# Kernel tuning notes

Hardware: AMD Instinct MI355X
Metric: run time of the kernel (lower is better)

Reference implementation:

```python
import jax, jax.numpy as jnp
import numpy as np

H = 2048      # hidden_size
E = 16        # num_experts
I = 512       # moe_intermediate_size
IS = 2048     # shared_expert_intermediate_size
TOP_K = 2
B, S = 1, 2048


def setup_inputs() -> dict:
    key = jax.random.key(0)
    ks = jax.random.split(key, 9)
    std = 0.02
    return {
        "hidden_states": jax.random.normal(ks[0], (B, S, H), dtype=jnp.float32),
        "gate_w": jax.random.normal(ks[1], (E, H), dtype=jnp.float32) * std,
        "w1": jax.random.normal(ks[2], (E, I, H), dtype=jnp.float32) * std,  # gate_proj per expert
        "w2": jax.random.normal(ks[3], (E, H, I), dtype=jnp.float32) * std,  # down_proj per expert
        "w3": jax.random.normal(ks[4], (E, I, H), dtype=jnp.float32) * std,  # up_proj per expert
        "ws_gate": jax.random.normal(ks[5], (IS, H), dtype=jnp.float32) * std,  # shared gate_proj
        "ws_up": jax.random.normal(ks[6], (IS, H), dtype=jnp.float32) * std,    # shared up_proj
        "ws_down": jax.random.normal(ks[7], (H, IS), dtype=jnp.float32) * std,  # shared down_proj
        "shared_gate_w": jax.random.normal(ks[8], (1, H), dtype=jnp.float32) * std,
    }


def reference(hidden_states, gate_w, w1, w2, w3, ws_gate, ws_up, ws_down, shared_gate_w):
    b, s, h = hidden_states.shape
    x = hidden_states.reshape(-1, h)                     # [T, H]
    T = x.shape[0]

    # Router: softmax in fp32, top-k, renormalize (norm_topk_prob=True)
    router_logits = x @ gate_w.T                         # [T, E]
    routing = jax.nn.softmax(router_logits.astype(jnp.float32), axis=-1)
    topw, sel = jax.lax.top_k(routing, TOP_K)            # [T, K]
    topw = topw / jnp.sum(topw, axis=-1, keepdims=True)
    topw = topw.astype(x.dtype)

    # Scatter top-k weights into dense [T, E] combine matrix (torch_moe semantics)
    combine = jnp.zeros((T, E), dtype=x.dtype).at[jnp.arange(T)[:, None], sel].set(topw)

    # Expert SwiGLU MLPs evaluated densely, masked/weighted by combine
    hmid = jax.nn.silu(jnp.einsum('th,eih->tei', x, w1)) * jnp.einsum('th,eih->tei', x, w3)  # [T,E,I]
    hmid = hmid * combine[:, :, None]
    moe_out = jnp.einsum('tei,ehi->th', hmid, w2)        # [T, H]

    # Shared expert with sigmoid gate
    shared = (jax.nn.silu(x @ ws_gate.T) * (x @ ws_up.T)) @ ws_down.T  # [T, H]
    shared = jax.nn.sigmoid(x @ shared_gate_w.T) * shared

    return (moe_out + shared).reshape(b, s, h)
```

## Files before the change

kernel.cpp:

```cpp
#include <hip/hip_runtime.h>
#include <hip/hip_bf16.h>
#include <cmath>

#define HDIM 2048
#define NEXP 16
#define IDIM 512
#define ISDIM 2048
#define NTOK 2048
#define MAXTILES 80
#define ROWSCAP (MAXTILES * 64)
#define NB_EXP 640
#define NB_SH 1024

typedef short bf16x8 __attribute__((ext_vector_type(8)));
typedef float f32x4 __attribute__((ext_vector_type(4)));

__device__ __forceinline__ unsigned short f2bf(float f) {
  unsigned int u = __builtin_bit_cast(unsigned int, f);
  u += 0x7FFFu + ((u >> 16) & 1u);
  return (unsigned short)(u >> 16);
}

__device__ __forceinline__ void stage_w8(const float* __restrict__ src,
                                         unsigned short* __restrict__ dst) {
  const float4* p = reinterpret_cast<const float4*>(src);
  float4 a = p[0];
  float4 b = p[1];
  bf16x8 v = {(short)f2bf(a.x), (short)f2bf(a.y), (short)f2bf(a.z), (short)f2bf(a.w),
              (short)f2bf(b.x), (short)f2bf(b.y), (short)f2bf(b.z), (short)f2bf(b.w)};
  *reinterpret_cast<bf16x8*>(dst) = v;
}

__global__ __launch_bounds__(256) void k_router(const float* __restrict__ x,
                                                const float* __restrict__ gate_w,
                                                const float* __restrict__ sgw,
                                                unsigned short* __restrict__ xb,
                                                int* __restrict__ sel,
                                                float* __restrict__ wnorm,
                                                float* __restrict__ sig,
                                                int* __restrict__ counts) {
  __shared__ float lg[4][17];
  int tid = threadIdx.x, wid = tid >> 6, lane = tid & 63;
  int t = blockIdx.x * 4 + wid;
  const float4* xrow = reinterpret_cast<const float4*>(x + (size_t)t * HDIM);
  float4 xv[8];
#pragma unroll
  for (int s = 0; s < 8; s++) xv[s] = xrow[s * 64 + lane];
  ushort4* xbrow = reinterpret_cast<ushort4*>(xb + (size_t)t * HDIM);
#pragma unroll
  for (int s = 0; s < 8; s++) {
    ushort4 o;
    o.x = f2bf(xv[s].x); o.y = f2bf(xv[s].y); o.z = f2bf(xv[s].z); o.w = f2bf(xv[s].w);
    xbrow[s * 64 + lane] = o;
  }
#pragma unroll 1
  for (int e = 0; e < 17; e++) {
    const float4* gr =
        reinterpret_cast<const float4*>(e < 16 ? gate_w + (size_t)e * HDIM : sgw);
    float acc = 0.f;
#pragma unroll
    for (int s = 0; s < 8; s++) {
      float4 g = gr[s * 64 + lane];
      acc += xv[s].x * g.x + xv[s].y * g.y + xv[s].z * g.z + xv[s].w * g.w;
    }
#pragma unroll
    for (int off = 32; off; off >>= 1) acc += __shfl_xor(acc, off, 64);
    if (lane == 0) lg[wid][e] = acc;
  }
  if (lane == 0) {
    float* L = lg[wid];
    int i1 = 0; float v1 = L[0];
    for (int i = 1; i < NEXP; i++) if (L[i] > v1) { v1 = L[i]; i1 = i; }
    int i2 = (i1 == 0) ? 1 : 0; float v2 = L[i2];
    for (int i = 0; i < NEXP; i++)
      if (i != i1 && i != i2 && L[i] > v2) { v2 = L[i]; i2 = i; }
    float wa = 1.f / (1.f + expf(v2 - v1));
    sel[2 * t] = i1; sel[2 * t + 1] = i2;
    wnorm[2 * t] = wa; wnorm[2 * t + 1] = 1.f - wa;
    sig[t] = 1.f / (1.f + expf(-L[16]));
    atomicAdd(&counts[i1], 1);
    atomicAdd(&counts[i2], 1);
  }
}

__global__ __launch_bounds__(256) void k_scan_scatter(const int* __restrict__ counts,
                                                      const int* __restrict__ sel,
                                                      int* __restrict__ tile_expert,
                                                      int* __restrict__ row_token,
                                                      int* __restrict__ tok2row) {
  __shared__ int offs_s[NEXP];
  __shared__ int fill_s[NEXP];
  int tid = threadIdx.x;
  for (int r = tid; r < ROWSCAP; r += 256) row_token[r] = -1;
  if (tid < NEXP) fill_s[tid] = 0;
  if (tid == 0) {
    int acc = 0;
    for (int e = 0; e < NEXP; e++) {
      offs_s[e] = acc;
      int nt = (counts[e] + 63) >> 6;
      for (int i = 0; i < nt; i++) tile_expert[(acc >> 6) + i] = e;
      acc += nt << 6;
    }
    for (int m = acc >> 6; m < MAXTILES; m++) tile_expert[m] = -1;
  }
  __syncthreads();
  for (int t = tid; t < NTOK; t += 256) {
    for (int k = 0; k < 2; k++) {
      int e = sel[2 * t + k];
      int pos = atomicAdd(&fill_s[e], 1);
      int row = offs_s[e] + pos;
      row_token[row] = t;
      tok2row[2 * t + k] = row;
    }
  }
}

__global__ __launch_bounds__(256) void k_gu(
    const unsigned short* __restrict__ xb, const float* __restrict__ w1,
    const float* __restrict__ w3, const float* __restrict__ wsg,
    const float* __restrict__ wsu, const int* __restrict__ tile_expert,
    const int* __restrict__ row_token, unsigned short* __restrict__ hmid,
    unsigned short* __restrict__ hs) {
  __shared__ unsigned short As[64 * 72];
  __shared__ unsigned short Bg[64 * 72];
  __shared__ unsigned short Bu[64 * 72];
  __shared__ int toks[64];
  int bid = blockIdx.x, tid = threadIdx.x;
  const float *bGp, *bUp;
  unsigned short* outp;
  int ostride, mt, ncol;
  if (bid < NB_EXP) {
    mt = bid >> 3;
    int nt = bid & 7;
    int e = tile_expert[mt];
    if (e < 0) return;
    if (tid < 64) {
      int tk = row_token[mt * 64 + tid];
      toks[tid] = tk < 0 ? 0 : tk;
    }
    bGp = w1 + ((size_t)e * IDIM + nt * 64) * HDIM;
    bUp = w3 + ((size_t)e * IDIM + nt * 64) * HDIM;
    outp = hmid; ostride = IDIM; ncol = nt * 64;
  } else {
    int sb = bid - NB_EXP;
    mt = sb >> 5;
    int nt = sb & 31;
    if (tid < 64) toks[tid] = mt * 64 + tid;
    bGp = wsg + (size_t)(nt * 64) * HDIM;
    bUp = wsu + (size_t)(nt * 64) * HDIM;
    outp = hs; ostride = ISDIM; ncol = nt * 64;
  }
  int wave = tid >> 6, lane = tid & 63;
  int wm = wave >> 1, wn = wave & 1;
  int quad = lane >> 4, l16 = lane & 15;
  int r0 = tid >> 3, kof0 = (tid & 7) << 3;
  int c2 = tid + 256;
  int r1 = c2 >> 3, kof1 = (c2 & 7) << 3;
  f32x4 accG[2][2] = {};
  f32x4 accU[2][2] = {};
  __syncthreads();
  for (int k0 = 0; k0 < HDIM; k0 += 64) {
    *reinterpret_cast<bf16x8*>(&As[r0 * 72 + kof0]) =
        *reinterpret_cast<const bf16x8*>(xb + (size_t)toks[r0] * HDIM + k0 + kof0);
    *reinterpret_cast<bf16x8*>(&As[r1 * 72 + kof1]) =
        *reinterpret_cast<const bf16x8*>(xb + (size_t)toks[r1] * HDIM + k0 + kof1);
    stage_w8(bGp + (size_t)r0 * HDIM + k0 + kof0, &Bg[r0 * 72 + kof0]);
    stage_w8(bGp + (size_t)r1 * HDIM + k0 + kof1, &Bg[r1 * 72 + kof1]);
    stage_w8(bUp + (size_t)r0 * HDIM + k0 + kof0, &Bu[r0 * 72 + kof0]);
    stage_w8(bUp + (size_t)r1 * HDIM + k0 + kof1, &Bu[r1 * 72 + kof1]);
    __syncthreads();
#pragma unroll
    for (int ks = 0; ks < 2; ks++) {
      bf16x8 af[2], bg[2], bu[2];
#pragma unroll
      for (int ms = 0; ms < 2; ms++)
        af[ms] = *reinterpret_cast<const bf16x8*>(
            &As[(wm * 32 + ms * 16 + l16) * 72 + ks * 32 + quad * 8]);
#pragma unroll
      for (int ns = 0; ns < 2; ns++) {
        bg[ns] = *reinterpret_cast<const bf16x8*>(
            &Bg[(wn * 32 + ns * 16 + l16) * 72 + ks * 32 + quad * 8]);
        bu[ns] = *reinterpret_cast<const bf16x8*>(
            &Bu[(wn * 32 + ns * 16 + l16) * 72 + ks * 32 + quad * 8]);
      }
#pragma unroll
      for (int ms = 0; ms < 2; ms++)
#pragma unroll
        for (int ns = 0; ns < 2; ns++) {
          accG[ms][ns] = __builtin_amdgcn_mfma_f32_16x16x32_bf16(af[ms], bg[ns], accG[ms][ns], 0, 0, 0);
          accU[ms][ns] = __builtin_amdgcn_mfma_f32_16x16x32_bf16(af[ms], bu[ns], accU[ms][ns], 0, 0, 0);
        }
    }
    __syncthreads();
  }
#pragma unroll
  for (int ms = 0; ms < 2; ms++)
#pragma unroll
    for (int ns = 0; ns < 2; ns++)
#pragma unroll
      for (int r = 0; r < 4; r++) {
        float g = accG[ms][ns][r], u = accU[ms][ns][r];
        float hv = (g / (1.f + __expf(-g))) * u;
        int row = mt * 64 + wm * 32 + ms * 16 + quad * 4 + r;
        int col = ncol + wn * 32 + ns * 16 + l16;
        outp[(size_t)row * ostride + col] = f2bf(hv);
      }
}

__global__ __launch_bounds__(256) void k_expert_down(
    const unsigned short* __restrict__ hmid, const float* __restrict__ w2,
    const int* __restrict__ tile_expert, float* __restrict__ moe_rows) {
  int mt = blockIdx.y, nt = blockIdx.x;
  int e = tile_expert[mt];
  if (e < 0) return;
  __shared__ unsigned short As[64 * 72];
  __shared__ unsigned short Bs[64 * 72];
  int tid = threadIdx.x;
  const float* w2e = w2 + ((size_t)e * HDIM + nt * 64) * IDIM;
  int wave = tid >> 6, lane = tid & 63;
  int wm = wave >> 1, wn = wave & 1;
  int quad = lane >> 4, l16 = lane & 15;
  int r0 = tid >> 3, kof0 = (tid & 7) << 3;
  int c2 = tid + 256;
  int r1 = c2 >> 3, kof1 = (c2 & 7) << 3;
  f32x4 acc[2][2] = {};
  for (int k0 = 0; k0 < IDIM; k0 += 64) {
    *reinterpret_cast<bf16x8*>(&As[r0 * 72 + kof0]) =
        *reinterpret_cast<const bf16x8*>(hmid + (size_t)(mt * 64 + r0) * IDIM + k0 + kof0);
    *reinterpret_cast<bf16x8*>(&As[r1 * 72 + kof1]) =
        *reinterpret_cast<const bf16x8*>(hmid + (size_t)(mt * 64 + r1) * IDIM + k0 + kof1);
    stage_w8(w2e + (size_t)r0 * IDIM + k0 + kof0, &Bs[r0 * 72 + kof0]);
    stage_w8(w2e + (size_t)r1 * IDIM + k0 + kof1, &Bs[r1 * 72 + kof1]);
    __syncthreads();
#pragma unroll
    for (int ks = 0; ks < 2; ks++) {
      bf16x8 af[2], bf[2];
#pragma unroll
      for (int ms = 0; ms < 2; ms++)
        af[ms] = *reinterpret_cast<const bf16x8*>(
            &As[(wm * 32 + ms * 16 + l16) * 72 + ks * 32 + quad * 8]);
#pragma unroll
      for (int ns = 0; ns < 2; ns++)
        bf[ns] = *reinterpret_cast<const bf16x8*>(
            &Bs[(wn * 32 + ns * 16 + l16) * 72 + ks * 32 + quad * 8]);
#pragma unroll
      for (int ms = 0; ms < 2; ms++)
#pragma unroll
        for (int ns = 0; ns < 2; ns++)
          acc[ms][ns] = __builtin_amdgcn_mfma_f32_16x16x32_bf16(af[ms], bf[ns], acc[ms][ns], 0, 0, 0);
    }
    __syncthreads();
  }
#pragma unroll
  for (int ms = 0; ms < 2; ms++)
#pragma unroll
    for (int ns = 0; ns < 2; ns++)
#pragma unroll
      for (int r = 0; r < 4; r++) {
        int row = mt * 64 + wm * 32 + ms * 16 + quad * 4 + r;
        int col = nt * 64 + wn * 32 + ns * 16 + l16;
        moe_rows[(size_t)row * HDIM + col] = acc[ms][ns][r];
      }
}

__global__ __launch_bounds__(256) void k_shared_down(
    const unsigned short* __restrict__ hs, const float* __restrict__ wsd,
    const float* __restrict__ moe_rows, const int* __restrict__ tok2row,
    const float* __restrict__ wnorm, const float* __restrict__ sig,
    float* __restrict__ out) {
  int mt = blockIdx.y, nt = blockIdx.x;
  __shared__ unsigned short As[64 * 72];
  __shared__ unsigned short Bs[64 * 72];
  int tid = threadIdx.x;
  const float* wsde = wsd + (size_t)(nt * 64) * ISDIM;
  int wave = tid >> 6, lane = tid & 63;
  int wm = wave >> 1, wn = wave & 1;
  int quad = lane >> 4, l16 = lane & 15;
  int r0 = tid >> 3, kof0 = (tid & 7) << 3;
  int c2 = tid + 256;
  int r1 = c2 >> 3, kof1 = (c2 & 7) << 3;
  f32x4 acc[2][2] = {};
  for (int k0 = 0; k0 < ISDIM; k0 += 64) {
    *reinterpret_cast<bf16x8*>(&As[r0 * 72 + kof0]) =
        *reinterpret_cast<const bf16x8*>(hs + (size_t)(mt * 64 + r0) * ISDIM + k0 + kof0);
    *reinterpret_cast<bf16x8*>(&As[r1 * 72 + kof1]) =
        *reinterpret_cast<const bf16x8*>(hs + (size_t)(mt * 64 + r1) * ISDIM + k0 + kof1);
    stage_w8(wsde + (size_t)r0 * ISDIM + k0 + kof0, &Bs[r0 * 72 + kof0]);
    stage_w8(wsde + (size_t)r1 * ISDIM + k0 + kof1, &Bs[r1 * 72 + kof1]);
    __syncthreads();
#pragma unroll
    for (int ks = 0; ks < 2; ks++) {
      bf16x8 af[2], bf[2];
#pragma unroll
      for (int ms = 0; ms < 2; ms++)
        af[ms] = *reinterpret_cast<const bf16x8*>(
            &As[(wm * 32 + ms * 16 + l16) * 72 + ks * 32 + quad * 8]);
#pragma unroll
      for (int ns = 0; ns < 2; ns++)
        bf[ns] = *reinterpret_cast<const bf16x8*>(
            &Bs[(wn * 32 + ns * 16 + l16) * 72 + ks * 32 + quad * 8]);
#pragma unroll
      for (int ms = 0; ms < 2; ms++)
#pragma unroll
        for (int ns = 0; ns < 2; ns++)
          acc[ms][ns] = __builtin_amdgcn_mfma_f32_16x16x32_bf16(af[ms], bf[ns], acc[ms][ns], 0, 0, 0);
    }
    __syncthreads();
  }
#pragma unroll
  for (int ms = 0; ms < 2; ms++)
#pragma unroll
    for (int ns = 0; ns < 2; ns++)
#pragma unroll
      for (int r = 0; r < 4; r++) {
        int t = mt * 64 + wm * 32 + ms * 16 + quad * 4 + r;
        int col = nt * 64 + wn * 32 + ns * 16 + l16;
        float v = acc[ms][ns][r] * sig[t];
        int ra = tok2row[t * 2], rb = tok2row[t * 2 + 1];
        v += wnorm[t * 2] * moe_rows[(size_t)ra * HDIM + col] +
             wnorm[t * 2 + 1] * moe_rows[(size_t)rb * HDIM + col];
        out[(size_t)t * HDIM + col] = v;
      }
}

extern "C" void kernel_launch(void* const* d_in, const int* in_sizes, int n_in,
                              void* d_out, int out_size, void* d_ws, size_t ws_size,
                              hipStream_t stream) {
  const float* x = (const float*)d_in[0];
  const float* gate_w = (const float*)d_in[1];
  const float* w1 = (const float*)d_in[2];
  const float* w2 = (const float*)d_in[3];
  const float* w3 = (const float*)d_in[4];
  const float* wsg = (const float*)d_in[5];
  const float* wsu = (const float*)d_in[6];
  const float* wsd = (const float*)d_in[7];
  const float* sgw = (const float*)d_in[8];
  float* out = (float*)d_out;

  unsigned short* xb = (unsigned short*)d_ws;
  unsigned short* hs = xb + (size_t)NTOK * HDIM;
  unsigned short* hmid = hs + (size_t)NTOK * ISDIM;
  float* moe_rows = (float*)(hmid + (size_t)ROWSCAP * IDIM);
  float* wnorm = moe_rows + (size_t)ROWSCAP * HDIM;
  float* sig = wnorm + 2 * NTOK;
  int* sel = (int*)(sig + NTOK);
  int* tok2row = sel + 2 * NTOK;
  int* row_token = tok2row + 2 * NTOK;
  int* counts = row_token + ROWSCAP;
  int* tile_expert = counts + NEXP;

  hipMemsetAsync(counts, 0, NEXP * sizeof(int), stream);
  k_router<<<dim3(NTOK / 4), dim3(256), 0, stream>>>(x, gate_w, sgw, xb, sel, wnorm,
                                                     sig, counts);
  k_scan_scatter<<<dim3(1), dim3(256), 0, stream>>>(counts, sel, tile_expert,
                                                    row_token, tok2row);
  k_gu<<<dim3(NB_EXP + NB_SH), dim3(256), 0, stream>>>(xb, w1, w3, wsg, wsu,
                                                       tile_expert, row_token, hmid, hs);
  k_expert_down<<<dim3(HDIM / 64, MAXTILES), dim3(256), 0, stream>>>(
      hmid, w2, tile_expert, moe_rows);
  k_shared_down<<<dim3(HDIM / 64, NTOK / 64), dim3(256), 0, stream>>>(
      hs, wsd, moe_rows, tok2row, wnorm, sig, out);
}
```

Measured before the change: 482.4 us.

## Pre-convert weights to bf16, enlarge GEMM tiles, use direct-to-LDS loads and atomic combine

Adds a kernel that converts all expert and shared weights to bf16 once per call, so the GEMM kernels stop converting fp32 weights during staging and the weights are reread in half the size. The gate/up and down GEMMs get larger N tiles (128 and 256), XOR-swizzled LDS layouts without padding, and global_load_lds for the B operand. Expert-down and shared-down are merged into one kernel that scatters weighted results into a zeroed output with float atomics, removing the moe_rows intermediate buffer. The extra conversion pass reads and writes about 360 MB every call, and the atomics make summation order nondeterministic.

```diff
diff --git a/kernel.cpp b/kernel.cpp
--- a/kernel.cpp
+++ b/kernel.cpp
@@ -9,32 +9,53 @@
 #define NTOK 2048
 #define MAXTILES 80
 #define ROWSCAP (MAXTILES * 64)
-#define NB_EXP 640
-#define NB_SH 1024
+
+#define GU_NBLK_EXP (MAXTILES * 4)
+#define GU_NBLK_SH ((NTOK / 64) * (ISDIM / 128))
+#define DN_NBLK_EXP (MAXTILES * 8)
+#define DN_NBLK_SH ((NTOK / 64) * (HDIM / 256))
 
 typedef short bf16x8 __attribute__((ext_vector_type(8)));
 typedef float f32x4 __attribute__((ext_vector_type(4)));
-
-__device__ __forceinline__ unsigned short f2bf(float f) {
+typedef unsigned short us;
+typedef __attribute__((address_space(1))) const unsigned int* as1p;
+typedef __attribute__((address_space(3))) unsigned int* as3p;
+
+__device__ __forceinline__ us f2bf(float f) {
   unsigned int u = __builtin_bit_cast(unsigned int, f);
   u += 0x7FFFu + ((u >> 16) & 1u);
-  return (unsigned short)(u >> 16);
-}
-
-__device__ __forceinline__ void stage_w8(const float* __restrict__ src,
-                                         unsigned short* __restrict__ dst) {
-  const float4* p = reinterpret_cast<const float4*>(src);
-  float4 a = p[0];
-  float4 b = p[1];
+  return (us)(u >> 16);
+}
+
+__device__ __forceinline__ void glds16(const void* g, void* l) {
+  __builtin_amdgcn_global_load_lds((as1p)(unsigned long long)g,
+                                   (as3p)(unsigned int)(unsigned long long)l, 16, 0, 0);
+}
+
+struct SrcPtrs { const float* p[6]; };
+__global__ __launch_bounds__(256) void k_convert(SrcPtrs s, us* __restrict__ dst) {
+  int b = blockIdx.x;
+  const float* sp;
+  long long rel;
+  size_t doff;
+  if (b < 8192)       { sp = s.p[0]; rel = b;         doff = 0; }
+  else if (b < 16384) { sp = s.p[1]; rel = b - 8192;  doff = 16777216; }
+  else if (b < 24576) { sp = s.p[2]; rel = b - 16384; doff = 33554432; }
+  else if (b < 26624) { sp = s.p[3]; rel = b - 24576; doff = 50331648; }
+  else if (b < 28672) { sp = s.p[4]; rel = b - 26624; doff = 54525952; }
+  else                { sp = s.p[5]; rel = b - 28672; doff = 58720256; }
+  size_t i8 = (size_t)rel * 2048 + threadIdx.x * 8;
+  float4 a = ((const float4*)sp)[i8 >> 2];
+  float4 c = ((const float4*)sp)[(i8 >> 2) + 1];
   bf16x8 v = {(short)f2bf(a.x), (short)f2bf(a.y), (short)f2bf(a.z), (short)f2bf(a.w),
-              (short)f2bf(b.x), (short)f2bf(b.y), (short)f2bf(b.z), (short)f2bf(b.w)};
-  *reinterpret_cast<bf16x8*>(dst) = v;
+              (short)f2bf(c.x), (short)f2bf(c.y), (short)f2bf(c.z), (short)f2bf(c.w)};
+  *(bf16x8*)(dst + doff + i8) = v;
 }
 
 __global__ __launch_bounds__(256) void k_router(const float* __restrict__ x,
                                                 const float* __restrict__ gate_w,
                                                 const float* __restrict__ sgw,
-                                                unsigned short* __restrict__ xb,
+                                                us* __restrict__ xb,
                                                 int* __restrict__ sel,
                                                 float* __restrict__ wnorm,
                                                 float* __restrict__ sig,
@@ -85,9 +106,10 @@
 
 __global__ __launch_bounds__(256) void k_scan_scatter(const int* __restrict__ counts,
                                                       const int* __restrict__ sel,
+                                                      const float* __restrict__ wnorm,
                                                       int* __restrict__ tile_expert,
                                                       int* __restrict__ row_token,
-                                                      int* __restrict__ tok2row) {
+                                                      float* __restrict__ rw) {
   __shared__ int offs_s[NEXP];
   __shared__ int fill_s[NEXP];
   int tid = threadIdx.x;
@@ -110,81 +132,80 @@
       int pos = atomicAdd(&fill_s[e], 1);
       int row = offs_s[e] + pos;
       row_token[row] = t;
-      tok2row[2 * t + k] = row;
+      rw[row] = wnorm[2 * t + k];
     }
   }
 }
 
 __global__ __launch_bounds__(256) void k_gu(
-    const unsigned short* __restrict__ xb, const float* __restrict__ w1,
-    const float* __restrict__ w3, const float* __restrict__ wsg,
-    const float* __restrict__ wsu, const int* __restrict__ tile_expert,
-    const int* __restrict__ row_token, unsigned short* __restrict__ hmid,
-    unsigned short* __restrict__ hs) {
-  __shared__ unsigned short As[64 * 72];
-  __shared__ unsigned short Bg[64 * 72];
-  __shared__ unsigned short Bu[64 * 72];
-  __shared__ int toks[64];
+    const us* __restrict__ xb, const us* __restrict__ wb1, const us* __restrict__ wb3,
+    const us* __restrict__ wsgb, const us* __restrict__ wsub,
+    const int* __restrict__ tile_expert, const int* __restrict__ row_token,
+    us* __restrict__ hmid, us* __restrict__ hs) {
+  __shared__ us As[64 * 64];
+  __shared__ us Bg[128 * 64];
+  __shared__ us Bu[128 * 64];
   int bid = blockIdx.x, tid = threadIdx.x;
-  const float *bGp, *bUp;
-  unsigned short* outp;
-  int ostride, mt, ncol;
-  if (bid < NB_EXP) {
-    mt = bid >> 3;
-    int nt = bid & 7;
+  int w = tid >> 6, lane = tid & 63;
+  const us *bG, *bU;
+  us* outp;
+  int mt, n0, ostride, tok0, tok1;
+  int r0 = tid >> 3;
+  if (bid < GU_NBLK_EXP) {
+    mt = bid >> 2; int nt = bid & 3;
     int e = tile_expert[mt];
     if (e < 0) return;
-    if (tid < 64) {
-      int tk = row_token[mt * 64 + tid];
-      toks[tid] = tk < 0 ? 0 : tk;
-    }
-    bGp = w1 + ((size_t)e * IDIM + nt * 64) * HDIM;
-    bUp = w3 + ((size_t)e * IDIM + nt * 64) * HDIM;
-    outp = hmid; ostride = IDIM; ncol = nt * 64;
+    int a = row_token[mt * 64 + r0];
+    int b = row_token[mt * 64 + r0 + 32];
+    tok0 = a < 0 ? 0 : a;
+    tok1 = b < 0 ? 0 : b;
+    bG = wb1 + ((size_t)e * IDIM + nt * 128) * HDIM;
+    bU = wb3 + ((size_t)e * IDIM + nt * 128) * HDIM;
+    outp = hmid; ostride = IDIM; n0 = nt * 128;
   } else {
-    int sb = bid - NB_EXP;
-    mt = sb >> 5;
-    int nt = sb & 31;
-    if (tid < 64) toks[tid] = mt * 64 + tid;
-    bGp = wsg + (size_t)(nt * 64) * HDIM;
-    bUp = wsu + (size_t)(nt * 64) * HDIM;
-    outp = hs; ostride = ISDIM; ncol = nt * 64;
-  }
-  int wave = tid >> 6, lane = tid & 63;
-  int wm = wave >> 1, wn = wave & 1;
-  int quad = lane >> 4, l16 = lane & 15;
-  int r0 = tid >> 3, kof0 = (tid & 7) << 3;
-  int c2 = tid + 256;
-  int r1 = c2 >> 3, kof1 = (c2 & 7) << 3;
-  f32x4 accG[2][2] = {};
-  f32x4 accU[2][2] = {};
-  __syncthreads();
+    int sb = bid - GU_NBLK_EXP;
+    mt = sb >> 4; int nt = sb & 15;
+    tok0 = mt * 64 + r0;
+    tok1 = tok0 + 32;
+    bG = wsgb + (size_t)(nt * 128) * HDIM;
+    bU = wsub + (size_t)(nt * 128) * HDIM;
+    outp = hs; ostride = ISDIM; n0 = nt * 128;
+  }
+  int quad = lane >> 4, l16 = lane & 15, sw = l16 & 7;
+  int cg = ((lane & 7) ^ (lane >> 3)) * 8;
+  const us* aSrc0 = xb + (size_t)tok0 * HDIM + ((tid & 7) ^ (r0 & 7)) * 8;
+  const us* aSrc1 = xb + (size_t)tok1 * HDIM + ((tid & 7) ^ (r0 & 7)) * 8;
+  size_t bLaneOff = (size_t)(lane >> 3) * HDIM + cg;
+  f32x4 accG[4][2] = {};
+  f32x4 accU[4][2] = {};
   for (int k0 = 0; k0 < HDIM; k0 += 64) {
-    *reinterpret_cast<bf16x8*>(&As[r0 * 72 + kof0]) =
-        *reinterpret_cast<const bf16x8*>(xb + (size_t)toks[r0] * HDIM + k0 + kof0);
-    *reinterpret_cast<bf16x8*>(&As[r1 * 72 + kof1]) =
-        *reinterpret_cast<const bf16x8*>(xb + (size_t)toks[r1] * HDIM + k0 + kof1);
-    stage_w8(bGp + (size_t)r0 * HDIM + k0 + kof0, &Bg[r0 * 72 + kof0]);
-    stage_w8(bGp + (size_t)r1 * HDIM + k0 + kof1, &Bg[r1 * 72 + kof1]);
-    stage_w8(bUp + (size_t)r0 * HDIM + k0 + kof0, &Bu[r0 * 72 + kof0]);
-    stage_w8(bUp + (size_t)r1 * HDIM + k0 + kof1, &Bu[r1 * 72 + kof1]);
+    ((bf16x8*)As)[tid] = *(const bf16x8*)(aSrc0 + k0);
+    ((bf16x8*)As)[tid + 256] = *(const bf16x8*)(aSrc1 + k0);
+#pragma unroll
+    for (int ii = 0; ii < 8; ii++) {
+      int i = w * 8 + ii;
+      int g = i & 15;
+      if (i < 16)
+        glds16(bG + (size_t)g * 8 * HDIM + bLaneOff + k0, &Bg[g * 64 * 8]);
+      else
+        glds16(bU + (size_t)g * 8 * HDIM + bLaneOff + k0, &Bu[g * 64 * 8]);
+    }
     __syncthreads();
 #pragma unroll
     for (int ks = 0; ks < 2; ks++) {
-      bf16x8 af[2], bg[2], bu[2];
-#pragma unroll
-      for (int ms = 0; ms < 2; ms++)
-        af[ms] = *reinterpret_cast<const bf16x8*>(
-            &As[(wm * 32 + ms * 16 + l16) * 72 + ks * 32 + quad * 8]);
+      int cb = (ks * 4 + quad) ^ sw;
+      bf16x8 af[4], bg[2], bu[2];
+#pragma unroll
+      for (int ms = 0; ms < 4; ms++)
+        af[ms] = *(const bf16x8*)&As[((ms * 16 + l16) * 8 + cb) * 8];
 #pragma unroll
       for (int ns = 0; ns < 2; ns++) {
-        bg[ns] = *reinterpret_cast<const bf16x8*>(
-            &Bg[(wn * 32 + ns * 16 + l16) * 72 + ks * 32 + quad * 8]);
-        bu[ns] = *reinterpret_cast<const bf16x8*>(
-            &Bu[(wn * 32 + ns * 16 + l16) * 72 + ks * 32 + quad * 8]);
+        int n = w * 32 + ns * 16 + l16;
+        bg[ns] = *(const bf16x8*)&Bg[(n * 8 + cb) * 8];
+        bu[ns] = *(const bf16x8*)&Bu[(n * 8 + cb) * 8];
       }
 #pragma unroll
-      for (int ms = 0; ms < 2; ms++)
+      for (int ms = 0; ms < 4; ms++)
 #pragma unroll
         for (int ns = 0; ns < 2; ns++) {
           accG[ms][ns] = __builtin_amdgcn_mfma_f32_16x16x32_bf16(af[ms], bg[ns], accG[ms][ns], 0, 0, 0);
@@ -194,133 +215,106 @@
     __syncthreads();
   }
 #pragma unroll
-  for (int ms = 0; ms < 2; ms++)
+  for (int ms = 0; ms < 4; ms++)
 #pragma unroll
     for (int ns = 0; ns < 2; ns++)
 #pragma unroll
       for (int r = 0; r < 4; r++) {
         float g = accG[ms][ns][r], u = accU[ms][ns][r];
         float hv = (g / (1.f + __expf(-g))) * u;
-        int row = mt * 64 + wm * 32 + ms * 16 + quad * 4 + r;
-        int col = ncol + wn * 32 + ns * 16 + l16;
+        int row = mt * 64 + ms * 16 + quad * 4 + r;
+        int col = n0 + w * 32 + ns * 16 + l16;
         outp[(size_t)row * ostride + col] = f2bf(hv);
       }
 }
 
-__global__ __launch_bounds__(256) void k_expert_down(
-    const unsigned short* __restrict__ hmid, const float* __restrict__ w2,
-    const int* __restrict__ tile_expert, float* __restrict__ moe_rows) {
-  int mt = blockIdx.y, nt = blockIdx.x;
-  int e = tile_expert[mt];
-  if (e < 0) return;
-  __shared__ unsigned short As[64 * 72];
-  __shared__ unsigned short Bs[64 * 72];
-  int tid = threadIdx.x;
-  const float* w2e = w2 + ((size_t)e * HDIM + nt * 64) * IDIM;
-  int wave = tid >> 6, lane = tid & 63;
-  int wm = wave >> 1, wn = wave & 1;
-  int quad = lane >> 4, l16 = lane & 15;
-  int r0 = tid >> 3, kof0 = (tid & 7) << 3;
-  int c2 = tid + 256;
-  int r1 = c2 >> 3, kof1 = (c2 & 7) << 3;
-  f32x4 acc[2][2] = {};
-  for (int k0 = 0; k0 < IDIM; k0 += 64) {
-    *reinterpret_cast<bf16x8*>(&As[r0 * 72 + kof0]) =
-        *reinterpret_cast<const bf16x8*>(hmid + (size_t)(mt * 64 + r0) * IDIM + k0 + kof0);
-    *reinterpret_cast<bf16x8*>(&As[r1 * 72 + kof1]) =
-        *reinterpret_cast<const bf16x8*>(hmid + (size_t)(mt * 64 + r1) * IDIM + k0 + kof1);
-    stage_w8(w2e + (size_t)r0 * IDIM + k0 + kof0, &Bs[r0 * 72 + kof0]);
-    stage_w8(w2e + (size_t)r1 * IDIM + k0 + kof1, &Bs[r1 * 72 + kof1]);
+__global__ __launch_bounds__(256) void k_down(
+    const us* __restrict__ hmid, const us* __restrict__ hs,
+    const us* __restrict__ wb2, const us* __restrict__ wsdb,
+    const int* __restrict__ tile_expert, const int* __restrict__ row_token,
+    const float* __restrict__ rw, const float* __restrict__ sig,
+    float* __restrict__ out) {
+  __shared__ us As[64 * 64];
+  __shared__ us Bs[256 * 64];
+  __shared__ int rt_s[64];
+  __shared__ float rw_s[64];
+  int bid = blockIdx.x, tid = threadIdx.x;
+  int w = tid >> 6, lane = tid & 63;
+  const us *aBase, *bBase;
+  int K, mt, n0;
+  if (bid < DN_NBLK_EXP) {
+    mt = bid >> 3; int nt = bid & 7;
+    int e = tile_expert[mt];
+    if (e < 0) return;
+    aBase = hmid + (size_t)mt * 64 * IDIM; K = IDIM;
+    bBase = wb2 + ((size_t)e * HDIM + nt * 256) * IDIM;
+    n0 = nt * 256;
+    if (tid < 64) {
+      int tk = row_token[mt * 64 + tid];
+      rt_s[tid] = tk;
+      rw_s[tid] = tk < 0 ? 0.f : rw[mt * 64 + tid];
+    }
+  } else {
+    int sb = bid - DN_NBLK_EXP;
+    mt = sb >> 3; int nt = sb & 7;
+    aBase = hs + (size_t)mt * 64 * ISDIM; K = ISDIM;
+    bBase = wsdb + (size_t)(nt * 256) * ISDIM;
+    n0 = nt * 256;
+    if (tid < 64) {
+      rt_s[tid] = mt * 64 + tid;
+      rw_s[tid] = sig[mt * 64 + tid];
+    }
+  }
+  int quad = lane >> 4, l16 = lane & 15, sw = l16 & 7;
+  int r0 = tid >> 3;
+  int cg = ((lane & 7) ^ (lane >> 3)) * 8;
+  const us* aSrc0 = aBase + (size_t)r0 * K + ((tid & 7) ^ (r0 & 7)) * 8;
+  const us* aSrc1 = aBase + (size_t)(r0 + 32) * K + ((tid & 7) ^ (r0 & 7)) * 8;
+  size_t bLaneOff = (size_t)(lane >> 3) * K + cg;
+  f32x4 acc[4][4] = {};
+  for (int k0 = 0; k0 < K; k0 += 64) {
+    ((bf16x8*)As)[tid] = *(const bf16x8*)(aSrc0 + k0);
+    ((bf16x8*)As)[tid + 256] = *(const bf16x8*)(aSrc1 + k0);
+#pragma unroll
+    for (int ii = 0; ii < 8; ii++) {
+      int g = w * 8 + ii;
+      glds16(bBase + (size_t)g * 8 * K + bLaneOff + k0, &Bs[g * 64 * 8]);
+    }
     __syncthreads();
 #pragma unroll
     for (int ks = 0; ks < 2; ks++) {
-      bf16x8 af[2], bf[2];
-#pragma unroll
-      for (int ms = 0; ms < 2; ms++)
-        af[ms] = *reinterpret_cast<const bf16x8*>(
-            &As[(wm * 32 + ms * 16 + l16) * 72 + ks * 32 + quad * 8]);
-#pragma unroll
-      for (int ns = 0; ns < 2; ns++)
-        bf[ns] = *reinterpret_cast<const bf16x8*>(
-            &Bs[(wn * 32 + ns * 16 + l16) * 72 + ks * 32 + quad * 8]);
-#pragma unroll
-      for (int ms = 0; ms < 2; ms++)
-#pragma unroll
-        for (int ns = 0; ns < 2; ns++)
+      int cb = (ks * 4 + quad) ^ sw;
+      bf16x8 af[4], bf[4];
+#pragma unroll
+      for (int ms = 0; ms < 4; ms++)
+        af[ms] = *(const bf16x8*)&As[((ms * 16 + l16) * 8 + cb) * 8];
+#pragma unroll
+      for (int ns = 0; ns < 4; ns++) {
+        int n = w * 64 + ns * 16 + l16;
+        bf[ns] = *(const bf16x8*)&Bs[(n * 8 + cb) * 8];
+      }
+#pragma unroll
+      for (int ms = 0; ms < 4; ms++)
+#pragma unroll
+        for (int ns = 0; ns < 4; ns++)
           acc[ms][ns] = __builtin_amdgcn_mfma_f32_16x16x32_bf16(af[ms], bf[ns], acc[ms][ns], 0, 0, 0);
     }
     __syncthreads();
   }
 #pragma unroll
-  for (int ms = 0; ms < 2; ms++)
-#pragma unroll
-    for (int ns = 0; ns < 2; ns++)
-#pragma unroll
-      for (int r = 0; r < 4; r++) {
-        int row = mt * 64 + wm * 32 + ms * 16 + quad * 4 + r;
-        int col = nt * 64 + wn * 32 + ns * 16 + l16;
-        moe_rows[(size_t)row * HDIM + col] = acc[ms][ns][r];
+  for (int ms = 0; ms < 4; ms++)
+#pragma unroll
+    for (int r = 0; r < 4; r++) {
+      int rr = ms * 16 + quad * 4 + r;
+      int tk = rt_s[rr];
+      float wgt = rw_s[rr];
+      if (tk >= 0) {
+        float* orow = out + (size_t)tk * HDIM + n0 + w * 64;
+#pragma unroll
+        for (int ns = 0; ns < 4; ns++)
+          atomicAdd(orow + ns * 16 + l16, wgt * acc[ms][ns][r]);
       }
-}
-
-__global__ __launch_bounds__(256) void k_shared_down(
-    const unsigned short* __restrict__ hs, const float* __restrict__ wsd,
-    const float* __restrict__ moe_rows, const int* __restrict__ tok2row,
-    const float* __restrict__ wnorm, const float* __restrict__ sig,
-    float* __restrict__ out) {
-  int mt = blockIdx.y, nt = blockIdx.x;
-  __shared__ unsigned short As[64 * 72];
-  __shared__ unsigned short Bs[64 * 72];
-  int tid = threadIdx.x;
-  const float* wsde = wsd + (size_t)(nt * 64) * ISDIM;
-  int wave = tid >> 6, lane = tid & 63;
-  int wm = wave >> 1, wn = wave & 1;
-  int quad = lane >> 4, l16 = lane & 15;
-  int r0 = tid >> 3, kof0 = (tid & 7) << 3;
-  int c2 = tid + 256;
-  int r1 = c2 >> 3, kof1 = (c2 & 7) << 3;
-  f32x4 acc[2][2] = {};
-  for (int k0 = 0; k0 < ISDIM; k0 += 64) {
-    *reinterpret_cast<bf16x8*>(&As[r0 * 72 + kof0]) =
-        *reinterpret_cast<const bf16x8*>(hs + (size_t)(mt * 64 + r0) * ISDIM + k0 + kof0);
-    *reinterpret_cast<bf16x8*>(&As[r1 * 72 + kof1]) =
-        *reinterpret_cast<const bf16x8*>(hs + (size_t)(mt * 64 + r1) * ISDIM + k0 + kof1);
-    stage_w8(wsde + (size_t)r0 * ISDIM + k0 + kof0, &Bs[r0 * 72 + kof0]);
-    stage_w8(wsde + (size_t)r1 * ISDIM + k0 + kof1, &Bs[r1 * 72 + kof1]);
-    __syncthreads();
-#pragma unroll
-    for (int ks = 0; ks < 2; ks++) {
-      bf16x8 af[2], bf[2];
-#pragma unroll
-      for (int ms = 0; ms < 2; ms++)
-        af[ms] = *reinterpret_cast<const bf16x8*>(
-            &As[(wm * 32 + ms * 16 + l16) * 72 + ks * 32 + quad * 8]);
-#pragma unroll
-      for (int ns = 0; ns < 2; ns++)
-        bf[ns] = *reinterpret_cast<const bf16x8*>(
-            &Bs[(wn * 32 + ns * 16 + l16) * 72 + ks * 32 + quad * 8]);
-#pragma unroll
-      for (int ms = 0; ms < 2; ms++)
-#pragma unroll
-        for (int ns = 0; ns < 2; ns++)
-          acc[ms][ns] = __builtin_amdgcn_mfma_f32_16x16x32_bf16(af[ms], bf[ns], acc[ms][ns], 0, 0, 0);
-    }
-    __syncthreads();
-  }
-#pragma unroll
-  for (int ms = 0; ms < 2; ms++)
-#pragma unroll
-    for (int ns = 0; ns < 2; ns++)
-#pragma unroll
-      for (int r = 0; r < 4; r++) {
-        int t = mt * 64 + wm * 32 + ms * 16 + quad * 4 + r;
-        int col = nt * 64 + wn * 32 + ns * 16 + l16;
-        float v = acc[ms][ns][r] * sig[t];
-        int ra = tok2row[t * 2], rb = tok2row[t * 2 + 1];
-        v += wnorm[t * 2] * moe_rows[(size_t)ra * HDIM + col] +
-             wnorm[t * 2 + 1] * moe_rows[(size_t)rb * HDIM + col];
-        out[(size_t)t * HDIM + col] = v;
-      }
+    }
 }
 
 extern "C" void kernel_launch(void* const* d_in, const int* in_sizes, int n_in,
@@ -337,27 +331,36 @@
   const float* sgw = (const float*)d_in[8];
   float* out = (float*)d_out;
 
-  unsigned short* xb = (unsigned short*)d_ws;
-  unsigned short* hs = xb + (size_t)NTOK * HDIM;
-  unsigned short* hmid = hs + (size_t)NTOK * ISDIM;
-  float* moe_rows = (float*)(hmid + (size_t)ROWSCAP * IDIM);
-  float* wnorm = moe_rows + (size_t)ROWSCAP * HDIM;
+  us* xb = (us*)d_ws;
+  us* hs = xb + (size_t)NTOK * HDIM;
+  us* hmid = hs + (size_t)NTOK * ISDIM;
+  us* wb1 = hmid + (size_t)ROWSCAP * IDIM;
+  us* wb3 = wb1 + (size_t)16777216;
+  us* wb2 = wb3 + (size_t)16777216;
+  us* wsgb = wb2 + (size_t)16777216;
+  us* wsub = wsgb + (size_t)4194304;
+  us* wsdb = wsub + (size_t)4194304;
+  float* rw = (float*)(wsdb + (size_t)4194304);
+  float* wnorm = rw + ROWSCAP;
   float* sig = wnorm + 2 * NTOK;
   int* sel = (int*)(sig + NTOK);
-  int* tok2row = sel + 2 * NTOK;
-  int* row_token = tok2row + 2 * NTOK;
+  int* row_token = sel + 2 * NTOK;
   int* counts = row_token + ROWSCAP;
   int* tile_expert = counts + NEXP;
 
+  SrcPtrs sp;
+  sp.p[0] = w1; sp.p[1] = w3; sp.p[2] = w2;
+  sp.p[3] = wsg; sp.p[4] = wsu; sp.p[5] = wsd;
+
   hipMemsetAsync(counts, 0, NEXP * sizeof(int), stream);
+  hipMemsetAsync(out, 0, (size_t)out_size * sizeof(float), stream);
+  k_convert<<<dim3(30720), dim3(256), 0, stream>>>(sp, wb1);
   k_router<<<dim3(NTOK / 4), dim3(256), 0, stream>>>(x, gate_w, sgw, xb, sel, wnorm,
                                                      sig, counts);
-  k_scan_scatter<<<dim3(1), dim3(256), 0, stream>>>(counts, sel, tile_expert,
-                                                    row_token, tok2row);
-  k_gu<<<dim3(NB_EXP + NB_SH), dim3(256), 0, stream>>>(xb, w1, w3, wsg, wsu,
-                                                       tile_expert, row_token, hmid, hs);
-  k_expert_down<<<dim3(HDIM / 64, MAXTILES), dim3(256), 0, stream>>>(
-      hmid, w2, tile_expert, moe_rows);
-  k_shared_down<<<dim3(HDIM / 64, NTOK / 64), dim3(256), 0, stream>>>(
-      hs, wsd, moe_rows, tok2row, wnorm, sig, out);
-}
+  k_scan_scatter<<<dim3(1), dim3(256), 0, stream>>>(counts, sel, wnorm, tile_expert,
+                                                    row_token, rw);
+  k_gu<<<dim3(GU_NBLK_EXP + GU_NBLK_SH), dim3(256), 0, stream>>>(
+      xb, wb1, wb3, wsgb, wsub, tile_expert, row_token, hmid, hs);
+  k_down<<<dim3(DN_NBLK_EXP + DN_NBLK_SH), dim3(256), 0, stream>>>(
+      hmid, hs, wb2, wsdb, tile_expert, row_token, rw, sig, out);
+}
```

Result: slower. 541.6 us (+12.3%).
